# Performance work log

Hardware: AMD Instinct MI355X
Metric: run time of the kernel (lower is better)

Reference implementation:

```python
import jax, jax.numpy as jnp
import numpy as np

EMB = 512
HEADS = 8
HEAD_DIM = EMB // HEADS


def setup_inputs() -> dict:
    key = jax.random.key(0)
    ks = jax.random.split(key, 6)
    b, t = 2, 4096
    x = jax.random.normal(ks[0], (b, t, EMB), dtype=jnp.float32)
    sc = 1.0 / np.sqrt(HEAD_DIM).astype(np.float32)
    Wq = jax.random.normal(ks[1], (HEAD_DIM, HEAD_DIM), dtype=jnp.float32) * sc
    Wk = jax.random.normal(ks[2], (HEAD_DIM, HEAD_DIM), dtype=jnp.float32) * sc
    Wv = jax.random.normal(ks[3], (HEAD_DIM, HEAD_DIM), dtype=jnp.float32) * sc
    Wu = jax.random.normal(ks[4], (EMB, EMB), dtype=jnp.float32) * (1.0 / np.sqrt(EMB).astype(np.float32))
    bu = jnp.zeros((EMB,), dtype=jnp.float32)
    return {"x": x, "Wq": Wq, "Wk": Wk, "Wv": Wv, "Wu": Wu, "bu": bu}


def reference(x, Wq, Wk, Wv, Wu, bu):
    b, t, e = x.shape
    s = Wq.shape[0]
    h = e // s
    xh = x.reshape(b, t, h, s)
    # torch Linear: y = x @ W.T (no bias for q/k/v)
    q = jnp.einsum('bthd,ed->bthe', xh, Wq)  # e here == s (head dim)
    k = jnp.einsum('bthd,ed->bthe', xh, Wk)
    v = jnp.einsum('bthd,ed->bthe', xh, Wv)
    # full [b,h,t,t] score matrix, scaled by sqrt(emb_dim) as in source
    dot = jnp.einsum('bqhd,bkhd->bhqk', q, k) / (e ** 0.5)
    att = jax.nn.softmax(dot, axis=-1)
    out = jnp.einsum('bhqk,bkhd->bqhd', att, v).reshape(b, t, e)
    return out @ Wu.T + bu
```

## Files before the change

### kernel.cpp

```cpp
#include <hip/hip_runtime.h>
#include <hip/hip_bf16.h>


#define T 4096
#define HEADS 8
#define HD 64
#define EMB 512
#define BATCH 2
#define BH (BATCH * HEADS)
#define NT (T / 64)

typedef __attribute__((ext_vector_type(8))) short short8;
typedef __attribute__((ext_vector_type(4))) short short4v;
typedef __attribute__((ext_vector_type(4))) float floatx4;

__device__ inline short f2bf(float f) {
  union { float f; unsigned u; } v; v.f = f;
  unsigned r = v.u + 0x7FFF + ((v.u >> 16) & 1);
  return (short)(r >> 16);
}

__device__ inline short8 pack8(float4 a, float4 b) {
  union { __hip_bfloat162 h[4]; short8 s; } u;
  float2 t;
  t.x = a.x; t.y = a.y; u.h[0] = __float22bfloat162_rn(t);
  t.x = a.z; t.y = a.w; u.h[1] = __float22bfloat162_rn(t);
  t.x = b.x; t.y = b.y; u.h[2] = __float22bfloat162_rn(t);
  t.x = b.z; t.y = b.w; u.h[3] = __float22bfloat162_rn(t);
  return u.s;
}

__device__ inline short4v pack4(floatx4 a) {
  union { __hip_bfloat162 h[2]; short4v s; } u;
  float2 t;
  t.x = a[0]; t.y = a[1]; u.h[0] = __float22bfloat162_rn(t);
  t.x = a[2]; t.y = a[3]; u.h[1] = __float22bfloat162_rn(t);
  return u.s;
}

__device__ inline short8 packbf(const float* p) {
  union { __hip_bfloat162 h[4]; short8 s; } u;
  float2 t;
  t.x = p[0]; t.y = p[1]; u.h[0] = __float22bfloat162_rn(t);
  t.x = p[2]; t.y = p[3]; u.h[1] = __float22bfloat162_rn(t);
  t.x = p[4]; t.y = p[5]; u.h[2] = __float22bfloat162_rn(t);
  t.x = p[6]; t.y = p[7]; u.h[3] = __float22bfloat162_rn(t);
  return u.s;
}

__device__ inline int swz(int row, int byte) {
  return (row * 128 + byte) ^ ((row & 7) << 4);
}

__global__ __launch_bounds__(256) void qkv_kernel(
    const float* __restrict__ x, const float* __restrict__ Wq,
    const float* __restrict__ Wk, const float* __restrict__ Wv,
    short* __restrict__ q_ws, short* __restrict__ k_ws, short* __restrict__ vt_ws) {
  __shared__ __align__(16) short xs[128 * 64];
  __shared__ __align__(16) short ob[128 * 64];
  const int tid = threadIdx.x;
  const int lane = tid & 63;
  const int w = tid >> 6;
  const int g = lane >> 4, lr = lane & 15;
  const long rowbase = (long)blockIdx.x * 128;
  const float c2 = 0.0441941738241592f * 1.4426950408889634f;

  {
    int row = tid >> 1, hf = tid & 1;
    const float4* xv = (const float4*)(x + (rowbase + row) * 64 + hf * 32);
#pragma unroll
    for (int c = 0; c < 4; ++c) {
      float4 a = xv[2 * c], b = xv[2 * c + 1];
      *(short8*)((char*)xs + swz(row, hf * 64 + c * 16)) = pack8(a, b);
    }
  }
  __syncthreads();

  const float* Ws[3] = {Wq, Wk, Wv};
  for (int m = 0; m < 3; ++m) {
    const float* W = Ws[m];
    const float sc = (m == 0) ? c2 : 1.0f;
    for (int nt = 0; nt < 4; ++nt) {
      const int coln_a = nt * 16 + lr;
      const float4* wr0 = (const float4*)(W + coln_a * 64 + 8 * g);
      const float4* wr1 = (const float4*)(W + coln_a * 64 + 32 + 8 * g);
      float4 w0 = wr0[0], w1 = wr0[1], w2 = wr1[0], w3 = wr1[1];
      w0.x *= sc; w0.y *= sc; w0.z *= sc; w0.w *= sc;
      w1.x *= sc; w1.y *= sc; w1.z *= sc; w1.w *= sc;
      w2.x *= sc; w2.y *= sc; w2.z *= sc; w2.w *= sc;
      w3.x *= sc; w3.y *= sc; w3.z *= sc; w3.w *= sc;
      short8 b0 = pack8(w0, w1);
      short8 b1 = pack8(w2, w3);
      for (int mr = 0; mr < 2; ++mr) {
        const int arow = w * 32 + mr * 16 + lr;
        short8 a0 = *(short8*)((char*)xs + swz(arow, g * 16));
        short8 a1 = *(short8*)((char*)xs + swz(arow, 64 + g * 16));
        floatx4 acc = 0;
        acc = __builtin_amdgcn_mfma_f32_16x16x32_bf16(b0, a0, acc, 0, 0, 0);
        acc = __builtin_amdgcn_mfma_f32_16x16x32_bf16(b1, a1, acc, 0, 0, 0);
        if (m < 2) {
          *(short4v*)((char*)ob + swz(w * 32 + mr * 16 + lr, 32 * nt + 8 * g)) = pack4(acc);
        } else {
          long R = rowbase + w * 32 + mr * 16 + lr;
          int bb = (int)(R >> 15);
          int h = (int)(R & 7);
          int t = (int)((R >> 3) & 4095);
          int tp = (t & ~31) | (((t >> 2) & 3) << 3) | (((t >> 4) & 1) << 2) | (t & 3);
          short4v pk = pack4(acc);
#pragma unroll
          for (int jj = 0; jj < 4; ++jj) {
            int coln = nt * 16 + 4 * g + jj;
            vt_ws[((long)(bb * HEADS + h) * 64 + coln) * T + tp] = pk[jj];
          }
        }
      }
    }
    if (m < 2) {
      short* dst_ws = (m == 0) ? q_ws : k_ws;
      __syncthreads();
      {
        int row = tid >> 1, hf = tid & 1;
        long R = rowbase + row;
        int bb = (int)(R >> 15);
        int h = (int)(R & 7);
        int t = (int)((R >> 3) & 4095);
        short* dst = dst_ws + ((long)(bb * HEADS + h) * T + t) * 64 + hf * 32;
#pragma unroll
        for (int c = 0; c < 4; ++c) {
          short8 v = *(short8*)((char*)ob + swz(row, hf * 64 + c * 16));
          *(short8*)(dst + c * 8) = v;
        }
      }
      __syncthreads();
    }
  }
}

__global__ __launch_bounds__(256) void attn_kernel(
    const short* __restrict__ q_ws, const short* __restrict__ k_ws,
    const short* __restrict__ vt_ws, short* __restrict__ o_ws) {
  __shared__ __align__(16) short Ks[2][64 * 64];
  __shared__ __align__(16) short Vs[2][64 * 64];
  const int tid = threadIdx.x, lane = tid & 63, w = tid >> 6;
  const int g = lane >> 4, lr = lane & 15;
  const int bh = blockIdx.y;
  const int q0 = blockIdx.x * 128;
  const short* Qp = q_ws + (long)bh * T * 64;
  const short* Kp = k_ws + (long)bh * T * 64;
  const short* Vt = vt_ws + (long)bh * 64 * T;

  short8 aq[2][2];
#pragma unroll
  for (int mt = 0; mt < 2; ++mt) {
    int r = q0 + w * 32 + mt * 16 + lr;
    aq[mt][0] = *(const short8*)(Qp + (long)r * 64 + g * 8);
    aq[mt][1] = *(const short8*)(Qp + (long)r * 64 + 32 + g * 8);
  }

  floatx4 acc[2][4];
#pragma unroll
  for (int mt = 0; mt < 2; ++mt)
#pragma unroll
    for (int dt = 0; dt < 4; ++dt) acc[mt][dt] = 0;
  float ellp[2] = {0.f, 0.f};

  const int srow = tid >> 2;
  const int sseg = (tid & 3) * 16;

  {
    const short8* ksrc = (const short8*)(Kp + (long)srow * 64 + sseg);
    short8 k0 = ksrc[0], k1 = ksrc[1];
    const short8* vsrc = (const short8*)(Vt + (long)srow * T + sseg);
    short8 v0 = vsrc[0], v1 = vsrc[1];
    *(short8*)((char*)Ks[0] + swz(srow, sseg * 2)) = k0;
    *(short8*)((char*)Ks[0] + swz(srow, sseg * 2 + 16)) = k1;
    *(short8*)((char*)Vs[0] + swz(srow, sseg * 2)) = v0;
    *(short8*)((char*)Vs[0] + swz(srow, sseg * 2 + 16)) = v1;
  }
  __syncthreads();

  for (int it = 0; it < NT; ++it) {
    const int cur = it & 1;
    const int nk = ((it + 1) & (NT - 1)) * 64;
    const short8* ksrc = (const short8*)(Kp + (long)(nk + srow) * 64 + sseg);
    short8 nk0 = ksrc[0], nk1 = ksrc[1];
    const short8* vsrc = (const short8*)(Vt + (long)srow * T + nk + sseg);
    short8 nv0 = vsrc[0], nv1 = vsrc[1];

    const char* KsB = (const char*)Ks[cur];
    const char* VsB = (const char*)Vs[cur];

    short8 kb[4][2], vb[4][2];
#pragma unroll
    for (int kt = 0; kt < 4; ++kt) {
      kb[kt][0] = *(const short8*)(KsB + swz(kt * 16 + lr, g * 16));
      kb[kt][1] = *(const short8*)(KsB + swz(kt * 16 + lr, 64 + g * 16));
    }
#pragma unroll
    for (int dt = 0; dt < 4; ++dt) {
      vb[dt][0] = *(const short8*)(VsB + swz(dt * 16 + lr, g * 16));
      vb[dt][1] = *(const short8*)(VsB + swz(dt * 16 + lr, 64 + g * 16));
    }

#pragma unroll
    for (int mt = 0; mt < 2; ++mt) {
      floatx4 s[4];
#pragma unroll
      for (int kt = 0; kt < 4; ++kt) {
        floatx4 z = {-3.f, -3.f, -3.f, -3.f};
        z = __builtin_amdgcn_mfma_f32_16x16x32_bf16(kb[kt][0], aq[mt][0], z, 0, 0, 0);
        z = __builtin_amdgcn_mfma_f32_16x16x32_bf16(kb[kt][1], aq[mt][1], z, 0, 0, 0);
        s[kt] = z;
      }
      float p[16];
#pragma unroll
      for (int kt = 0; kt < 4; ++kt)
#pragma unroll
        for (int r = 0; r < 4; ++r)
          p[kt * 4 + r] = __builtin_amdgcn_exp2f(s[kt][r]);
#pragma unroll
      for (int e = 0; e < 16; ++e) ellp[mt] += p[e];
      short8 pa0 = packbf(p);
      short8 pa1 = packbf(p + 8);
#pragma unroll
      for (int dt = 0; dt < 4; ++dt) {
        acc[mt][dt] = __builtin_amdgcn_mfma_f32_16x16x32_bf16(pa0, vb[dt][0], acc[mt][dt], 0, 0, 0);
        acc[mt][dt] = __builtin_amdgcn_mfma_f32_16x16x32_bf16(pa1, vb[dt][1], acc[mt][dt], 0, 0, 0);
      }
    }

    char* KsN = (char*)Ks[cur ^ 1];
    char* VsN = (char*)Vs[cur ^ 1];
    *(short8*)(KsN + swz(srow, sseg * 2)) = nk0;
    *(short8*)(KsN + swz(srow, sseg * 2 + 16)) = nk1;
    *(short8*)(VsN + swz(srow, sseg * 2)) = nv0;
    *(short8*)(VsN + swz(srow, sseg * 2 + 16)) = nv1;
    __syncthreads();
  }

  float ef[2];
#pragma unroll
  for (int mt = 0; mt < 2; ++mt) {
    float e = ellp[mt];
    e += __shfl_xor(e, 16);
    e += __shfl_xor(e, 32);
    ef[mt] = e;
  }
  const int bb = bh >> 3, h = bh & 7;
#pragma unroll
  for (int mt = 0; mt < 2; ++mt) {
#pragma unroll
    for (int j = 0; j < 4; ++j) {
      float rl = 1.0f / __shfl(ef[mt], 4 * g + j);
      int trow = q0 + w * 32 + mt * 16 + 4 * g + j;
      long ob2 = ((long)(bb * T + trow)) * EMB + h * 64;
#pragma unroll
      for (int dt = 0; dt < 4; ++dt)
        o_ws[ob2 + dt * 16 + lr] = f2bf(acc[mt][dt][j] * rl);
    }
  }
}

__global__ __launch_bounds__(256) void proj_kernel(
    const short* __restrict__ o_ws, const float* __restrict__ Wu,
    const float* __restrict__ bu, float* __restrict__ out) {
  __shared__ __align__(16) short As[64 * 64];
  __shared__ __align__(16) short Bs[128 * 64];
  const int tid = threadIdx.x;
  const int lane = tid & 63, w = tid >> 6;
  const int g = lane >> 4, lr = lane & 15;
  const int m0 = blockIdx.x * 64;
  const int n0 = blockIdx.y * 128;

  floatx4 acc[8];
#pragma unroll
  for (int nt = 0; nt < 8; ++nt) acc[nt] = 0;

  for (int kc = 0; kc < EMB; kc += 64) {
    {
      int row = tid >> 2, kp = (tid & 3) * 16;
      const short8* src = (const short8*)(o_ws + (long)(m0 + row) * EMB + kc + kp);
      short8 v0 = src[0], v1 = src[1];
      *(short8*)((char*)As + swz(row, kp * 2)) = v0;
      *(short8*)((char*)As + swz(row, kp * 2 + 16)) = v1;
    }
#pragma unroll
    for (int nn = 0; nn < 2; ++nn) {
      int n = nn * 64 + (tid >> 2), kp = (tid & 3) * 16;
      const float4* src = (const float4*)(Wu + (long)(n0 + n) * EMB + kc + kp);
      *(short8*)((char*)Bs + swz(n, kp * 2)) = pack8(src[0], src[1]);
      *(short8*)((char*)Bs + swz(n, kp * 2 + 16)) = pack8(src[2], src[3]);
    }
    __syncthreads();

    int arow = w * 16 + lr;
    short8 a0 = *(short8*)((char*)As + swz(arow, g * 16));
    short8 a1 = *(short8*)((char*)As + swz(arow, 64 + g * 16));
#pragma unroll
    for (int nt = 0; nt < 8; ++nt) {
      int n = nt * 16 + lr;
      short8 b0 = *(short8*)((char*)Bs + swz(n, g * 16));
      short8 b1 = *(short8*)((char*)Bs + swz(n, 64 + g * 16));
      acc[nt] = __builtin_amdgcn_mfma_f32_16x16x32_bf16(b0, a0, acc[nt], 0, 0, 0);
      acc[nt] = __builtin_amdgcn_mfma_f32_16x16x32_bf16(b1, a1, acc[nt], 0, 0, 0);
    }
    __syncthreads();
  }

  const int mrow = m0 + w * 16 + lr;
#pragma unroll
  for (int nt = 0; nt < 8; ++nt) {
    float4 bias = *(const float4*)(bu + n0 + nt * 16 + 4 * g);
    float4 o;
    o.x = acc[nt][0] + bias.x;
    o.y = acc[nt][1] + bias.y;
    o.z = acc[nt][2] + bias.z;
    o.w = acc[nt][3] + bias.w;
    *(float4*)(out + (long)mrow * EMB + n0 + nt * 16 + 4 * g) = o;
  }
}

extern "C" void kernel_launch(void* const* d_in, const int* in_sizes, int n_in,
                              void* d_out, int out_size, void* d_ws, size_t ws_size,
                              hipStream_t stream) {
  const float* x  = (const float*)d_in[0];
  const float* Wq = (const float*)d_in[1];
  const float* Wk = (const float*)d_in[2];
  const float* Wv = (const float*)d_in[3];
  const float* Wu = (const float*)d_in[4];
  const float* bu = (const float*)d_in[5];
  float* out = (float*)d_out;

  const long per = (long)BH * T * 64;
  short* q_ws  = (short*)d_ws;
  short* k_ws  = q_ws + per;
  short* vt_ws = k_ws + per;
  short* o_ws  = vt_ws + per;

  qkv_kernel<<<512, 256, 0, stream>>>(x, Wq, Wk, Wv, q_ws, k_ws, vt_ws);
  attn_kernel<<<dim3(T / 128, BH), 256, 0, stream>>>(q_ws, k_ws, vt_ws, o_ws);
  proj_kernel<<<dim3(BATCH * T / 64, EMB / 128), 256, 0, stream>>>(o_ws, Wu, bu, out);
}
```

Baseline: 128.8 us.

## Split attention KV range in two and merge partial outputs in new kernel

The attention kernel now splits each query tile's key/value range into two halves and launches 1024 blocks instead of 512. A block-index remap interleaves heads so neighbouring blocks work on different batch/head pairs. Each split writes its unnormalized bf16 accumulator and row sum to the workspace. A new merge kernel adds the two partials and normalizes them before the projection. The aim is more parallelism and better latency hiding on the GPU, paid for with an extra kernel launch, extra global-memory traffic for the partial outputs, and bf16 rounding of unnormalized values.

```diff
diff --git a/kernel.cpp b/kernel.cpp
--- a/kernel.cpp
+++ b/kernel.cpp
@@ -18,6 +18,11 @@
   union { float f; unsigned u; } v; v.f = f;
   unsigned r = v.u + 0x7FFF + ((v.u >> 16) & 1);
   return (short)(r >> 16);
+}
+
+__device__ inline float bf2f(short s) {
+  union { unsigned u; float f; } v; v.u = ((unsigned)(unsigned short)s) << 16;
+  return v.f;
 }
 
 __device__ inline short8 pack8(float4 a, float4 b) {
@@ -138,13 +143,17 @@
 
 __global__ __launch_bounds__(256) void attn_kernel(
     const short* __restrict__ q_ws, const short* __restrict__ k_ws,
-    const short* __restrict__ vt_ws, short* __restrict__ o_ws) {
+    const short* __restrict__ vt_ws, short* __restrict__ pacc,
+    float* __restrict__ ellw) {
   __shared__ __align__(16) short Ks[2][64 * 64];
   __shared__ __align__(16) short Vs[2][64 * 64];
   const int tid = threadIdx.x, lane = tid & 63, w = tid >> 6;
   const int g = lane >> 4, lr = lane & 15;
-  const int bh = blockIdx.y;
-  const int q0 = blockIdx.x * 128;
+  const int id = blockIdx.x;
+  const int bh = (id & 7) * 2 + ((id >> 3) & 1);
+  const int q0 = ((id >> 4) & 31) * 128;
+  const int split = (id >> 9) & 1;
+  const int kvbase = split * (T / 2);
   const short* Qp = q_ws + (long)bh * T * 64;
   const short* Kp = k_ws + (long)bh * T * 64;
   const short* Vt = vt_ws + (long)bh * 64 * T;
@@ -168,9 +177,9 @@
   const int sseg = (tid & 3) * 16;
 
   {
-    const short8* ksrc = (const short8*)(Kp + (long)srow * 64 + sseg);
+    const short8* ksrc = (const short8*)(Kp + (long)(kvbase + srow) * 64 + sseg);
     short8 k0 = ksrc[0], k1 = ksrc[1];
-    const short8* vsrc = (const short8*)(Vt + (long)srow * T + sseg);
+    const short8* vsrc = (const short8*)(Vt + (long)srow * T + kvbase + sseg);
     short8 v0 = vsrc[0], v1 = vsrc[1];
     *(short8*)((char*)Ks[0] + swz(srow, sseg * 2)) = k0;
     *(short8*)((char*)Ks[0] + swz(srow, sseg * 2 + 16)) = k1;
@@ -179,9 +188,9 @@
   }
   __syncthreads();
 
-  for (int it = 0; it < NT; ++it) {
+  for (int it = 0; it < 32; ++it) {
     const int cur = it & 1;
-    const int nk = ((it + 1) & (NT - 1)) * 64;
+    const int nk = kvbase + ((it + 1) & 31) * 64;
     const short8* ksrc = (const short8*)(Kp + (long)(nk + srow) * 64 + sseg);
     short8 nk0 = ksrc[0], nk1 = ksrc[1];
     const short8* vsrc = (const short8*)(Vt + (long)srow * T + nk + sseg);
@@ -247,18 +256,38 @@
     ef[mt] = e;
   }
   const int bb = bh >> 3, h = bh & 7;
+  short* pb = pacc + (long)split * 8192 * EMB;
 #pragma unroll
   for (int mt = 0; mt < 2; ++mt) {
+    if (g == 0)
+      ellw[((long)split * BH + bh) * T + q0 + w * 32 + mt * 16 + lr] = ef[mt];
 #pragma unroll
     for (int j = 0; j < 4; ++j) {
-      float rl = 1.0f / __shfl(ef[mt], 4 * g + j);
       int trow = q0 + w * 32 + mt * 16 + 4 * g + j;
       long ob2 = ((long)(bb * T + trow)) * EMB + h * 64;
 #pragma unroll
       for (int dt = 0; dt < 4; ++dt)
-        o_ws[ob2 + dt * 16 + lr] = f2bf(acc[mt][dt][j] * rl);
-    }
-  }
+        pb[ob2 + dt * 16 + lr] = f2bf(acc[mt][dt][j]);
+    }
+  }
+}
+
+__global__ __launch_bounds__(256) void merge_kernel(
+    short* __restrict__ pacc, const float* __restrict__ ellw) {
+  const long idx = (long)blockIdx.x * 256 + threadIdx.x;
+  const long e8 = idx * 8;
+  const int r = (int)(e8 >> 9);
+  const int c = (int)(e8 & 511);
+  const int b = r >> 12, t = r & 4095, h = c >> 6;
+  const int bh = b * HEADS + h;
+  float l = ellw[(long)bh * T + t] + ellw[((long)BH + bh) * T + t];
+  float rl = 1.0f / l;
+  short8 p0 = *(short8*)(pacc + e8);
+  short8 p1 = *(short8*)(pacc + (long)8192 * EMB + e8);
+  float o[8];
+#pragma unroll
+  for (int i = 0; i < 8; ++i) o[i] = (bf2f(p0[i]) + bf2f(p1[i])) * rl;
+  *(short8*)(pacc + e8) = packbf(o);
 }
 
 __global__ __launch_bounds__(256) void proj_kernel(
@@ -332,12 +361,15 @@
   float* out = (float*)d_out;
 
   const long per = (long)BH * T * 64;
+  const long osz = (long)8192 * EMB;
   short* q_ws  = (short*)d_ws;
   short* k_ws  = q_ws + per;
   short* vt_ws = k_ws + per;
-  short* o_ws  = vt_ws + per;
+  short* pacc  = vt_ws + per;
+  float* ellw  = (float*)(pacc + 2 * osz);
 
   qkv_kernel<<<512, 256, 0, stream>>>(x, Wq, Wk, Wv, q_ws, k_ws, vt_ws);
-  attn_kernel<<<dim3(T / 128, BH), 256, 0, stream>>>(q_ws, k_ws, vt_ws, o_ws);
-  proj_kernel<<<dim3(BATCH * T / 64, EMB / 128), 256, 0, stream>>>(o_ws, Wu, bu, out);
-}
+  attn_kernel<<<1024, 256, 0, stream>>>(q_ws, k_ws, vt_ws, pacc, ellw);
+  merge_kernel<<<(int)(osz / 8 / 256), 256, 0, stream>>>(pacc, ellw);
+  proj_kernel<<<dim3(BATCH * T / 64, EMB / 128), 256, 0, stream>>>(pacc, Wu, bu, out);
+}
```

Measured after the change: 136.4 us. +5.9%, slower.
